# Kernel optimization log

Measured on AMD Instinct MI355X. Metric: run time of the kernel, lower is better.

Reference implementation:

```python
import jax, jax.numpy as jnp
import numpy as np

B, T, I, H = 2048, 512, 9, 56


def _lstm_layer(x, w_ih, w_hh, b_ih, b_hh):
    """Single LSTM layer, batch_first x: [B, T, in] -> [B, T, H].
    PyTorch gate order: i, f, g, o."""
    # Precompute input projections for all timesteps in one GEMM: [B, T, 4H]
    xp = jnp.einsum('bti,gi->btg', x, w_ih) + b_ih + b_hh
    xp_t = jnp.transpose(xp, (1, 0, 2))  # [T, B, 4H]
    h0 = jnp.zeros((x.shape[0], w_hh.shape[1]), dtype=x.dtype)
    c0 = jnp.zeros_like(h0)

    def step(carry, xt):
        h, c = carry
        gates = xt + h @ w_hh.T  # [B, 4H]
        i, f, g, o = jnp.split(gates, 4, axis=-1)
        i = jax.nn.sigmoid(i)
        f = jax.nn.sigmoid(f)
        g = jnp.tanh(g)
        o = jax.nn.sigmoid(o)
        c = f * c + i * g
        h = o * jnp.tanh(c)
        return (h, c), h

    _, hs = jax.lax.scan(step, (h0, c0), xp_t)  # hs: [T, B, H]
    return jnp.transpose(hs, (1, 0, 2))  # [B, T, H]


def setup_inputs() -> dict:
    key = jax.random.key(0)
    ks = jax.random.split(key, 13)
    s_in = 1.0 / np.sqrt(H)
    inp = {
        'x': jax.random.normal(ks[0], (B, T, I), dtype=jnp.float32),
        'w_ih0': jax.random.uniform(ks[1], (4 * H, I), jnp.float32, -s_in, s_in),
        'w_hh0': jax.random.uniform(ks[2], (4 * H, H), jnp.float32, -s_in, s_in),
        'b_ih0': jax.random.uniform(ks[3], (4 * H,), jnp.float32, -s_in, s_in),
        'b_hh0': jax.random.uniform(ks[4], (4 * H,), jnp.float32, -s_in, s_in),
        'w_ih1': jax.random.uniform(ks[5], (4 * H, H), jnp.float32, -s_in, s_in),
        'w_hh1': jax.random.uniform(ks[6], (4 * H, H), jnp.float32, -s_in, s_in),
        'b_ih1': jax.random.uniform(ks[7], (4 * H,), jnp.float32, -s_in, s_in),
        'b_hh1': jax.random.uniform(ks[8], (4 * H,), jnp.float32, -s_in, s_in),
        'fc1_w': jax.random.uniform(ks[9], (H // 2, H), jnp.float32, -s_in, s_in),
        'fc1_b': jax.random.uniform(ks[10], (H // 2,), jnp.float32, -s_in, s_in),
        'fc2_w': jax.random.uniform(ks[11], (1, H // 2), jnp.float32, -0.2, 0.2),
        'fc2_b': jax.random.uniform(ks[12], (1,), jnp.float32, -0.2, 0.2),
    }
    return inp


def reference(x, w_ih0, w_hh0, b_ih0, b_hh0, w_ih1, w_hh1, b_ih1, b_hh1,
              fc1_w, fc1_b, fc2_w, fc2_b):
    h = _lstm_layer(x, w_ih0, w_hh0, b_ih0, b_hh0)   # [B, T, H]
    h = _lstm_layer(h, w_ih1, w_hh1, b_ih1, b_hh1)   # [B, T, H]
    last = h[:, -1]                                   # [B, H]
    y = jax.nn.relu(last @ fc1_w.T + fc1_b)           # [B, H//2]
    return y @ fc2_w.T + fc2_b                        # [B, 1]
```

## Files before the change

kernel.cpp:

```cpp
#include <hip/hip_runtime.h>
#include <stdint.h>

#define T_LEN 512
#define IN0   9
#define H     56
#define BG    8
#define NW    14
#define NTH   (NW * 64)
#define NBLK  256

typedef __attribute__((ext_vector_type(8))) short bfrag;
typedef __attribute__((ext_vector_type(4))) float ffrag;

#define MFMA(a,b,c) __builtin_amdgcn_mfma_f32_16x16x32_bf16((a),(b),(c),0,0,0)

__device__ __forceinline__ uint32_t bf16hi(float x) {
  uint32_t u = __float_as_uint(x);
  return (u + 0x7FFFu + ((u >> 16) & 1u)) & 0xFFFF0000u;
}
__device__ __forceinline__ void split_bf16(float x, short& hs, short& ls) {
  uint32_t hb = bf16hi(x);
  float lf = x - __uint_as_float(hb);
  hs = (short)(hb >> 16);
  ls = (short)(bf16hi(lf) >> 16);
}
__device__ __forceinline__ void split_bf16t(float x, short& hs, short& ls) {
  uint32_t hb = bf16hi(x);
  float lf = x - __uint_as_float(hb);
  hs = (short)(hb >> 16);
  ls = (short)(__float_as_uint(lf) >> 16);
}
__device__ __forceinline__ float dpp8(float v) {
  return __int_as_float(__builtin_amdgcn_update_dpp(0, __float_as_int(v), 0x128, 0xF, 0xF, true));
}
__device__ __forceinline__ float rcp_f(float v)  { return __builtin_amdgcn_rcpf(v); }
__device__ __forceinline__ float sigm_f(float v) { return rcp_f(1.0f + __expf(-v)); }
__device__ __forceinline__ float tanh_f(float v) { return 1.0f - 2.0f * rcp_f(1.0f + __expf(2.0f * v)); }

__global__ __launch_bounds__(NTH, 4)
void lstm_mfma10(const float* __restrict__ x,
                 const float* __restrict__ w_ih0, const float* __restrict__ w_hh0,
                 const float* __restrict__ b_ih0, const float* __restrict__ b_hh0,
                 const float* __restrict__ w_ih1, const float* __restrict__ w_hh1,
                 const float* __restrict__ b_ih1, const float* __restrict__ b_hh1,
                 const float* __restrict__ fc1_w, const float* __restrict__ fc1_b,
                 const float* __restrict__ fc2_w, const float* __restrict__ fc2_b,
                 float* __restrict__ out)
{
  __shared__ __align__(16) short hbufS[4 * 1024];
  __shared__ __align__(16) short xfS[T_LEN * 128];
  __shared__ __align__(16) float x8S[T_LEN * BG];
  __shared__ float sF[BG * H];
  __shared__ float sY[BG * 28];

  const int tid  = threadIdx.x;
  const int lane = tid & 63;
  const int w    = tid >> 6;
  const int c16  = lane & 15;
  const int quad = lane >> 4;

  const int np   = 16 * w + c16;
  const int jb   = np >> 2, gb = np & 3;
  const int wrow = gb * H + jb;

  for (int i = tid; i < 2048; i += NTH) ((int*)hbufS)[i] = 0;

  bfrag B0h[2], B0l[2], Buh[2], Bhh[2];
  #pragma unroll
  for (int s = 0; s < 2; ++s) {
    union { short sh[8]; bfrag v; } a0h, a0l, auh, ahh;
    #pragma unroll
    for (int jj = 0; jj < 8; ++jj) {
      const int k = 32 * s + quad * 8 + jj;
      const float w0 = (k < H) ? w_hh0[wrow * H + k] : w_ih0[wrow * IN0 + (k - 56)];
      const float wu = (k < H) ? w_ih1[wrow * H + k] : 0.0f;
      const float wh = (k < H) ? w_hh1[wrow * H + k] : 0.0f;
      split_bf16(w0, a0h.sh[jj], a0l.sh[jj]);
      short dum;
      split_bf16(wu, auh.sh[jj], dum);
      split_bf16(wh, ahh.sh[jj], dum);
    }
    B0h[s] = a0h.v; B0l[s] = a0l.v;
    Buh[s] = auh.v; Bhh[s] = ahh.v;
  }

  const int j4 = 4 * w + quad;
  ffrag bias0f, bias1f;
  #pragma unroll
  for (int r = 0; r < 4; ++r) {
    const float v0 = b_ih0[r * H + j4] + b_hh0[r * H + j4];
    const float v1 = b_ih1[r * H + j4] + b_hh1[r * H + j4];
    bias0f[r] = (c16 < 8) ? v0 : 0.0f;
    bias1f[r] = (c16 < 8) ? v1 : 0.0f;
  }
  const ffrag zerof = { 0.f, 0.f, 0.f, 0.f };

  const int lay = (lane >> 3) & 1;
  const int b   = lane & 7;
  float wx8a[4];
  #pragma unroll
  for (int r = 0; r < 4; ++r)
    wx8a[r] = lay ? w_ih0[(r * H + j4) * IN0 + 8] : 0.0f;

  const int kk   = j4 & 31;
  const int offE = (j4 >> 5) * 512 + ((kk >> 3) * 16 + b) * 8 + (kk & 7);
  short* const hp0 = hbufS + (lay ? 0 : 3 * 1024) + offE;
  short* const hp1 = hbufS + (lay ? 1 * 1024 : 2 * 1024) + offE;

  for (int item = tid; item < T_LEN * BG; item += NTH) {
    const int t  = item & (T_LEN - 1);
    const int bb = item >> 9;
    const float* xr = x + ((size_t)(blockIdx.x * BG + bb) * T_LEN + t) * IN0;
    union { short s[8]; bfrag v; } hi, lo;
    #pragma unroll
    for (int q = 0; q < 8; ++q) split_bf16t(xr[q], hi.s[q], lo.s[q]);
    *(bfrag*)((char*)xfS + (size_t)t * 256 + bb * 16)       = hi.v;
    *(bfrag*)((char*)xfS + (size_t)t * 256 + (bb + 8) * 16) = lo.v;
    x8S[t * 8 + bb] = xr[8];
  }

  const char* const hB = (const char*)hbufS;
  const char* const pU0_0 = hB + 2048 + lane * 16;
  const char* const pU0_1 = hB +        lane * 16;
  const char* const pH0_0 = hB + 4096 + lane * 16;
  const char* const pH1_0 = hB + 5120 + lane * 16;
  const char* const pH0_1 = hB + 6144 + lane * 16;
  const char* const pH1_1 = hB + 7168 + lane * 16;
  const char* pU1_0 = (quad == 3) ? ((const char*)xfS + 256 * 1 + c16 * 16)
                                  : (hB + 3072 + lane * 16);
  const char* pU1_1 = (quad == 3) ? ((const char*)xfS + 256 * 2 + c16 * 16)
                                  : (hB + 1024 + lane * 16);
  const char* px8_0 = (const char*)x8S + 32 * 1 + b * 4;
  const char* px8_1 = (const char*)x8S + 32 * 2 + b * 4;
  const int incU1 = (quad == 3) ? 512 : 0;

  float cst = 0.f;
  __syncthreads();

  {
    const bfrag U0 = *(const bfrag*)(hB + lane * 16);
    const char* pU1p = (quad == 3) ? ((const char*)xfS + c16 * 16)
                                   : (hB + 1024 + lane * 16);
    const bfrag U1 = *(const bfrag*)pU1p;
    const float x8v = x8S[b];
    ffrag a0 = MFMA(B0h[0], U0, bias0f);
    a0 = MFMA(B0h[1], U1, a0);
    a0 = MFMA(B0l[0], U0, a0);
    a0 = MFMA(B0l[1], U1, a0);
    float s0[4];
    #pragma unroll
    for (int r = 0; r < 4; ++r) s0[r] = a0[r] + dpp8(a0[r]);
    if (lay) {
      const float gi = fmaf(wx8a[0], x8v, s0[0]);
      const float gf = fmaf(wx8a[1], x8v, s0[1]);
      const float gg = fmaf(wx8a[2], x8v, s0[2]);
      const float go = fmaf(wx8a[3], x8v, s0[3]);
      const float iv = sigm_f(gi), fv = sigm_f(gf);
      const float gv = tanh_f(gg), ov = sigm_f(go);
      cst = fmaf(fv, cst, iv * gv);
      const float hv = ov * tanh_f(cst);
      short hs, hl; split_bf16t(hv, hs, hl);
      hp1[0] = hs; hp1[64] = hl;
    }
    __syncthreads();
  }

#define REGION(RR, L0PART, LASTR)                                               \
  {                                                                             \
    const bfrag U0 = *(const bfrag*)pU0_##RR;                                   \
    const bfrag U1 = *(const bfrag*)pU1_##RR;                                   \
    const bfrag H0 = *(const bfrag*)pH0_##RR;                                   \
    const bfrag H1 = *(const bfrag*)pH1_##RR;                                   \
    ffrag a0a, a0b;                                                             \
    float x8v = 0.0f;                                                           \
    if (L0PART) x8v = *(const float*)px8_##RR;                                  \
    __builtin_amdgcn_s_setprio(1);                                              \
    if (L0PART) {                                                               \
                           \
      a0a = MFMA(B0h[0], U0, bias0f);                                           \
      a0b = MFMA(B0l[0], U0, zerof);                                            \
      a0a = MFMA(B0h[1], U1, a0a);                                              \
      a0b = MFMA(B0l[1], U1, a0b);                                              \
    }                                                                           \
          \
    ffrag aH = MFMA(Bhh[0], H0, bias1f);                                        \
    aH = MFMA(Bhh[1], H1, aH);                                                  \
    aH = MFMA(Buh[0], U0, aH);                                                  \
    aH = MFMA(Buh[1], U1, aH);                                                  \
    __builtin_amdgcn_s_setprio(0);                                              \
    if (!LASTR) {                                                               \
      \
      float sv[4];                                                              \
      _Pragma("unroll")                                                         \
      for (int r = 0; r < 4; ++r) {                                             \
        const float t0 = a0a[r] + a0b[r];                                       \
        const float uu = lay ? t0 : aH[r];                                      \
        const float vv = lay ? aH[r] : t0;                                      \
        sv[r] = uu + dpp8(vv);                                                  \
      }                                                                         \
      const float gi = fmaf(wx8a[0], x8v, sv[0]);                               \
      const float gf = fmaf(wx8a[1], x8v, sv[1]);                               \
      const float gg = fmaf(wx8a[2], x8v, sv[2]);                               \
      const float go = fmaf(wx8a[3], x8v, sv[3]);                               \
      const float iv = sigm_f(gi), fv = sigm_f(gf);                             \
      const float gv = tanh_f(gg), ov = sigm_f(go);                             \
      cst = fmaf(fv, cst, iv * gv);                                             \
      const float hv = ov * tanh_f(cst);                                        \
      short hs, hl; split_bf16t(hv, hs, hl);                                    \
      short* hb2 = (RR == 0) ? hp0 : hp1;                                       \
      hb2[0] = hs; hb2[64] = hl;                                                \
    } else {                                                                    \
      float s1[4];                                                              \
      _Pragma("unroll")                                                         \
      for (int r = 0; r < 4; ++r) s1[r] = aH[r] + dpp8(aH[r]);                  \
      if (lay == 0) {                                                           \
        const float iv = sigm_f(s1[0]), fv = sigm_f(s1[1]);                     \
        const float gv = tanh_f(s1[2]), ov = sigm_f(s1[3]);                     \
        cst = fmaf(fv, cst, iv * gv);                                           \
        sF[b * H + j4] = ov * tanh_f(cst);                                      \
      }                                                                         \
    }                                                                           \
    __syncthreads();                                                            \
  }

  for (int it = 0; it < 255; ++it) {
    REGION(0, 1, 0)
    REGION(1, 1, 0)
    pU1_0 += incU1; pU1_1 += incU1;
    px8_0 += 64;    px8_1 += 64;
  }
  REGION(0, 1, 0)
  pU1_1 -= incU1;
  REGION(1, 0, 1)
#undef REGION

  if (tid < 28 * BG) {
    const int m  = tid >> 3;
    const int bb = tid & 7;
    float acc = fc1_b[m];
    const float4* w4 = (const float4*)(fc1_w + m * H);
    const float4* h4 = (const float4*)(sF + bb * H);
    #pragma unroll
    for (int qq = 0; qq < H / 4; ++qq) {
      const float4 wv4 = w4[qq], hv4 = h4[qq];
      acc = fmaf(wv4.x, hv4.x, acc);
      acc = fmaf(wv4.y, hv4.y, acc);
      acc = fmaf(wv4.z, hv4.z, acc);
      acc = fmaf(wv4.w, hv4.w, acc);
    }
    sY[bb * 28 + m] = fmaxf(acc, 0.0f);
  }
  __syncthreads();
  if (tid < BG) {
    float acc = fc2_b[0];
    #pragma unroll
    for (int m = 0; m < 28; ++m)
      acc = fmaf(fc2_w[m], sY[tid * 28 + m], acc);
    out[blockIdx.x * BG + tid] = acc;
  }
}

extern "C" void kernel_launch(void* const* d_in, const int* in_sizes, int n_in,
                              void* d_out, int out_size, void* d_ws, size_t ws_size,
                              hipStream_t stream)
{
  const float* x     = (const float*)d_in[0];
  const float* w_ih0 = (const float*)d_in[1];
  const float* w_hh0 = (const float*)d_in[2];
  const float* b_ih0 = (const float*)d_in[3];
  const float* b_hh0 = (const float*)d_in[4];
  const float* w_ih1 = (const float*)d_in[5];
  const float* w_hh1 = (const float*)d_in[6];
  const float* b_ih1 = (const float*)d_in[7];
  const float* b_hh1 = (const float*)d_in[8];
  const float* fc1_w = (const float*)d_in[9];
  const float* fc1_b = (const float*)d_in[10];
  const float* fc2_w = (const float*)d_in[11];
  const float* fc2_b = (const float*)d_in[12];
  float* out = (float*)d_out;

  lstm_mfma10<<<NBLK, NTH, 0, stream>>>(
      x, w_ih0, w_hh0, b_ih0, b_hh0, w_ih1, w_hh1, b_ih1, b_hh1,
      fc1_w, fc1_b, fc2_w, fc2_b, out);
}
```

Baseline: 425.8 us.

## Cut waves per block from 14 to 8, each handling two gate slices

Each block now runs 8 wavefronts instead of 14. Waves 0-5 each own two 16-column weight slices (the second is slice 8+w), and waves 6-7 own one. The MFMA and activation work per wave roughly doubles for most waves, in exchange for fewer waves taking part in each per-timestep __syncthreads barrier and less per-block scheduling overhead. The costs are higher register pressure, since weight fragments are duplicated, and load imbalance between waves with one and two slices on the serial recurrence path.

```diff
diff --git a/kernel.cpp b/kernel.cpp
--- a/kernel.cpp
+++ b/kernel.cpp
@@ -5,7 +5,7 @@
 #define IN0   9
 #define H     56
 #define BG    8
-#define NW    14
+#define NW    8
 #define NTH   (NW * 64)
 #define NBLK  256
 
@@ -37,8 +37,8 @@
 __device__ __forceinline__ float sigm_f(float v) { return rcp_f(1.0f + __expf(-v)); }
 __device__ __forceinline__ float tanh_f(float v) { return 1.0f - 2.0f * rcp_f(1.0f + __expf(2.0f * v)); }
 
-__global__ __launch_bounds__(NTH, 4)
-void lstm_mfma10(const float* __restrict__ x,
+__global__ __launch_bounds__(NTH, 2)
+void lstm_mfma12(const float* __restrict__ x,
                  const float* __restrict__ w_ih0, const float* __restrict__ w_hh0,
                  const float* __restrict__ b_ih0, const float* __restrict__ b_hh0,
                  const float* __restrict__ w_ih1, const float* __restrict__ w_hh1,
@@ -59,53 +59,72 @@
   const int c16  = lane & 15;
   const int quad = lane >> 4;
 
-  const int np   = 16 * w + c16;
-  const int jb   = np >> 2, gb = np & 3;
-  const int wrow = gb * H + jb;
+  const bool HASB = (w < 6);
+  const int  sBi  = HASB ? (8 + w) : 0;
 
   for (int i = tid; i < 2048; i += NTH) ((int*)hbufS)[i] = 0;
-
-  bfrag B0h[2], B0l[2], Buh[2], Bhh[2];
-  #pragma unroll
-  for (int s = 0; s < 2; ++s) {
-    union { short sh[8]; bfrag v; } a0h, a0l, auh, ahh;
-    #pragma unroll
-    for (int jj = 0; jj < 8; ++jj) {
-      const int k = 32 * s + quad * 8 + jj;
-      const float w0 = (k < H) ? w_hh0[wrow * H + k] : w_ih0[wrow * IN0 + (k - 56)];
-      const float wu = (k < H) ? w_ih1[wrow * H + k] : 0.0f;
-      const float wh = (k < H) ? w_hh1[wrow * H + k] : 0.0f;
-      split_bf16(w0, a0h.sh[jj], a0l.sh[jj]);
-      short dum;
-      split_bf16(wu, auh.sh[jj], dum);
-      split_bf16(wh, ahh.sh[jj], dum);
-    }
-    B0h[s] = a0h.v; B0l[s] = a0l.v;
-    Buh[s] = auh.v; Bhh[s] = ahh.v;
-  }
-
-  const int j4 = 4 * w + quad;
-  ffrag bias0f, bias1f;
-  #pragma unroll
-  for (int r = 0; r < 4; ++r) {
-    const float v0 = b_ih0[r * H + j4] + b_hh0[r * H + j4];
-    const float v1 = b_ih1[r * H + j4] + b_hh1[r * H + j4];
-    bias0f[r] = (c16 < 8) ? v0 : 0.0f;
-    bias1f[r] = (c16 < 8) ? v1 : 0.0f;
-  }
-  const ffrag zerof = { 0.f, 0.f, 0.f, 0.f };
 
   const int lay = (lane >> 3) & 1;
   const int b   = lane & 7;
-  float wx8a[4];
-  #pragma unroll
-  for (int r = 0; r < 4; ++r)
-    wx8a[r] = lay ? w_ih0[(r * H + j4) * IN0 + 8] : 0.0f;
-
-  const int kk   = j4 & 31;
-  const int offE = (j4 >> 5) * 512 + ((kk >> 3) * 16 + b) * 8 + (kk & 7);
-  short* const hp0 = hbufS + (lay ? 0 : 3 * 1024) + offE;
-  short* const hp1 = hbufS + (lay ? 1 * 1024 : 2 * 1024) + offE;
+
+  bfrag B0hA[2], B0lA[2], BuhA[2], BhhA[2];
+  bfrag B0hB[2], B0lB[2], BuhB[2], BhhB[2];
+
+#define LOADA(SUF, SIDX)                                                        \
+  {                                                                             \
+    const int np_ = 16 * (SIDX) + c16;                                          \
+    const int jb_ = np_ >> 2, gb_ = np_ & 3;                                    \
+    const int wrow_ = gb_ * H + jb_;                                            \
+    _Pragma("unroll")                                                           \
+    for (int s = 0; s < 2; ++s) {                                               \
+      union { short sh[8]; bfrag v; } a0h, a0l, auh, ahh;                       \
+      _Pragma("unroll")                                                         \
+      for (int jj = 0; jj < 8; ++jj) {                                          \
+        const int k = 32 * s + quad * 8 + jj;                                   \
+        const float w0 = (k < H) ? w_hh0[wrow_ * H + k]                         \
+                                 : w_ih0[wrow_ * IN0 + (k - 56)];               \
+        const float wu = (k < H) ? w_ih1[wrow_ * H + k] : 0.0f;                 \
+        const float wh = (k < H) ? w_hh1[wrow_ * H + k] : 0.0f;                 \
+        split_bf16(w0, a0h.sh[jj], a0l.sh[jj]);                                 \
+        short dum;                                                              \
+        split_bf16(wu, auh.sh[jj], dum);                       \
+        split_bf16(wh, ahh.sh[jj], dum);                                        \
+      }                                                                         \
+      B0h##SUF[s] = a0h.v; B0l##SUF[s] = a0l.v;                                 \
+      Buh##SUF[s] = auh.v; Bhh##SUF[s] = ahh.v;                                 \
+    }                                                                           \
+  }
+
+  LOADA(A, w)
+  LOADA(B, sBi)
+#undef LOADA
+
+  const int j4A = 4 * w + quad;
+  const int j4B = 4 * sBi + quad;
+  const ffrag zerof = { 0.f, 0.f, 0.f, 0.f };
+
+#define SETUPS(SUF, J4)                                                         \
+  ffrag bias0f##SUF, bias1f##SUF;                                               \
+  _Pragma("unroll")                                                             \
+  for (int r = 0; r < 4; ++r) {                                                 \
+    const float v0 = b_ih0[r * H + (J4)] + b_hh0[r * H + (J4)];                 \
+    const float v1 = b_ih1[r * H + (J4)] + b_hh1[r * H + (J4)];                 \
+    bias0f##SUF[r] = (c16 < 8) ? v0 : 0.0f;                                     \
+    bias1f##SUF[r] = (c16 < 8) ? v1 : 0.0f;                                     \
+  }                                                                             \
+  float wx8a##SUF[4];                                                           \
+  _Pragma("unroll")                                                             \
+  for (int r = 0; r < 4; ++r)                                                   \
+    wx8a##SUF[r] = lay ? w_ih0[(r * H + (J4)) * IN0 + 8] : 0.0f;                \
+  const int kk##SUF = (J4) & 31;                                                \
+  const int offE##SUF = ((J4) >> 5) * 512 + ((kk##SUF >> 3) * 16 + b) * 8       \
+                        + (kk##SUF & 7);                                        \
+  short* const hp0##SUF = hbufS + (lay ? 0 : 3 * 1024) + offE##SUF;             \
+  short* const hp1##SUF = hbufS + (lay ? 1 * 1024 : 2 * 1024) + offE##SUF;
+
+  SETUPS(A, j4A)
+  SETUPS(B, j4B)
+#undef SETUPS
 
   for (int item = tid; item < T_LEN * BG; item += NTH) {
     const int t  = item & (T_LEN - 1);
@@ -134,8 +153,62 @@
   const char* px8_1 = (const char*)x8S + 32 * 2 + b * 4;
   const int incU1 = (quad == 3) ? 512 : 0;
 
-  float cst = 0.f;
+  float cstA = 0.f, cstB = 0.f;
   __syncthreads();
+
+#define ACT0(A0, WX8, CST, HBP, X8V)                                            \
+  {                                                                             \
+    float s0[4];                                                                \
+    _Pragma("unroll")                                                           \
+    for (int r = 0; r < 4; ++r) s0[r] = A0[r] + dpp8(A0[r]);                    \
+    if (lay) {                                                                  \
+      const float gi = fmaf(WX8[0], X8V, s0[0]);                                \
+      const float gf = fmaf(WX8[1], X8V, s0[1]);                                \
+      const float gg = fmaf(WX8[2], X8V, s0[2]);                                \
+      const float go = fmaf(WX8[3], X8V, s0[3]);                                \
+      const float iv = sigm_f(gi), fv = sigm_f(gf);                             \
+      const float gv = tanh_f(gg), ov = sigm_f(go);                             \
+      CST = fmaf(fv, CST, iv * gv);                                             \
+      const float hv = ov * tanh_f(CST);                                        \
+      short hs, hl; split_bf16t(hv, hs, hl);                                    \
+      (HBP)[0] = hs; (HBP)[64] = hl;                                            \
+    }                                                                           \
+  }
+
+#define ACT1(A0A, A0B, AH, WX8, CST, HBP, X8V)                                  \
+  {                                                                             \
+    float sv[4];                                                                \
+    _Pragma("unroll")                                                           \
+    for (int r = 0; r < 4; ++r) {                                               \
+      const float t0 = A0A[r] + A0B[r];                                         \
+      const float uu = lay ? t0 : AH[r];                                        \
+      const float vv = lay ? AH[r] : t0;                                        \
+      sv[r] = uu + dpp8(vv);                                                    \
+    }                                                                           \
+    const float gi = fmaf(WX8[0], X8V, sv[0]);                                  \
+    const float gf = fmaf(WX8[1], X8V, sv[1]);                                  \
+    const float gg = fmaf(WX8[2], X8V, sv[2]);                                  \
+    const float go = fmaf(WX8[3], X8V, sv[3]);                                  \
+    const float iv = sigm_f(gi), fv = sigm_f(gf);                               \
+    const float gv = tanh_f(gg), ov = sigm_f(go);                               \
+    CST = fmaf(fv, CST, iv * gv);                                               \
+    const float hv = ov * tanh_f(CST);                                          \
+    short hs, hl; split_bf16t(hv, hs, hl);                                      \
+    (HBP)[0] = hs; (HBP)[64] = hl;                                              \
+  }
+
+#define ACTL(AH, CST, J4)                                                       \
+  {                                                                             \
+    float s1[4];                                                                \
+    _Pragma("unroll")                                                           \
+    for (int r = 0; r < 4; ++r) s1[r] = AH[r] + dpp8(AH[r]);                    \
+    if (lay == 0) {                                                             \
+      const float iv = sigm_f(s1[0]), fv = sigm_f(s1[1]);                       \
+      const float gv = tanh_f(s1[2]), ov = sigm_f(s1[3]);                       \
+      CST = fmaf(fv, CST, iv * gv);                                             \
+      sF[b * H + (J4)] = ov * tanh_f(CST);                                      \
+    }                                                                           \
+  }
 
   {
     const bfrag U0 = *(const bfrag*)(hB + lane * 16);
@@ -143,24 +216,17 @@
                                    : (hB + 1024 + lane * 16);
     const bfrag U1 = *(const bfrag*)pU1p;
     const float x8v = x8S[b];
-    ffrag a0 = MFMA(B0h[0], U0, bias0f);
-    a0 = MFMA(B0h[1], U1, a0);
-    a0 = MFMA(B0l[0], U0, a0);
-    a0 = MFMA(B0l[1], U1, a0);
-    float s0[4];
-    #pragma unroll
-    for (int r = 0; r < 4; ++r) s0[r] = a0[r] + dpp8(a0[r]);
-    if (lay) {
-      const float gi = fmaf(wx8a[0], x8v, s0[0]);
-      const float gf = fmaf(wx8a[1], x8v, s0[1]);
-      const float gg = fmaf(wx8a[2], x8v, s0[2]);
-      const float go = fmaf(wx8a[3], x8v, s0[3]);
-      const float iv = sigm_f(gi), fv = sigm_f(gf);
-      const float gv = tanh_f(gg), ov = sigm_f(go);
-      cst = fmaf(fv, cst, iv * gv);
-      const float hv = ov * tanh_f(cst);
-      short hs, hl; split_bf16t(hv, hs, hl);
-      hp1[0] = hs; hp1[64] = hl;
+    ffrag a0A = MFMA(B0hA[0], U0, bias0fA);
+    a0A = MFMA(B0hA[1], U1, a0A);
+    a0A = MFMA(B0lA[0], U0, a0A);
+    a0A = MFMA(B0lA[1], U1, a0A);
+    ACT0(a0A, wx8aA, cstA, hp1A, x8v)
+    if (HASB) {
+      ffrag a0B = MFMA(B0hB[0], U0, bias0fB);
+      a0B = MFMA(B0hB[1], U1, a0B);
+      a0B = MFMA(B0lB[0], U0, a0B);
+      a0B = MFMA(B0lB[1], U1, a0B);
+      ACT0(a0B, wx8aB, cstB, hp1B, x8v)
     }
     __syncthreads();
   }
@@ -171,54 +237,43 @@
     const bfrag U1 = *(const bfrag*)pU1_##RR;                                   \
     const bfrag H0 = *(const bfrag*)pH0_##RR;                                   \
     const bfrag H1 = *(const bfrag*)pH1_##RR;                                   \
-    ffrag a0a, a0b;                                                             \
+    ffrag a0aA, a0bA, a0aB, a0bB;                                               \
     float x8v = 0.0f;                                                           \
     if (L0PART) x8v = *(const float*)px8_##RR;                                  \
     __builtin_amdgcn_s_setprio(1);                                              \
     if (L0PART) {                                                               \
-                           \
-      a0a = MFMA(B0h[0], U0, bias0f);                                           \
-      a0b = MFMA(B0l[0], U0, zerof);                                            \
-      a0a = MFMA(B0h[1], U1, a0a);                                              \
-      a0b = MFMA(B0l[1], U1, a0b);                                              \
+      a0aA = MFMA(B0hA[0], U0, bias0fA);                                        \
+      a0bA = MFMA(B0lA[0], U0, zerof);                                          \
+      a0aA = MFMA(B0hA[1], U1, a0aA);                                           \
+      a0bA = MFMA(B0lA[1], U1, a0bA);                                           \
+      if (HASB) {                                                               \
+        a0aB = MFMA(B0hB[0], U0, bias0fB);                                      \
+        a0bB = MFMA(B0lB[0], U0, zerof);                                        \
+        a0aB = MFMA(B0hB[1], U1, a0aB);                                         \
+        a0bB = MFMA(B0lB[1], U1, a0bB);                                         \
+      }                                                                         \
     }                                                                           \
           \
-    ffrag aH = MFMA(Bhh[0], H0, bias1f);                                        \
-    aH = MFMA(Bhh[1], H1, aH);                                                  \
-    aH = MFMA(Buh[0], U0, aH);                                                  \
-    aH = MFMA(Buh[1], U1, aH);                                                  \
+    ffrag aHA = MFMA(BhhA[0], H0, bias1fA);                                     \
+    aHA = MFMA(BhhA[1], H1, aHA);                                               \
+    aHA = MFMA(BuhA[0], U0, aHA);                                               \
+    aHA = MFMA(BuhA[1], U1, aHA);                                               \
+    ffrag aHB;                                                                  \
+    if (HASB) {                                                                 \
+      aHB = MFMA(BhhB[0], H0, bias1fB);                                         \
+      aHB = MFMA(BhhB[1], H1, aHB);                                             \
+      aHB = MFMA(BuhB[0], U0, aHB);                                             \
+      aHB = MFMA(BuhB[1], U1, aHB);                                             \
+    }                                                                           \
     __builtin_amdgcn_s_setprio(0);                                              \
     if (!LASTR) {                                                               \
-      \
-      float sv[4];                                                              \
-      _Pragma("unroll")                                                         \
-      for (int r = 0; r < 4; ++r) {                                             \
-        const float t0 = a0a[r] + a0b[r];                                       \
-        const float uu = lay ? t0 : aH[r];                                      \
-        const float vv = lay ? aH[r] : t0;                                      \
-        sv[r] = uu + dpp8(vv);                                                  \
+      ACT1(a0aA, a0bA, aHA, wx8aA, cstA, ((RR) == 0) ? hp0A : hp1A, x8v)        \
+      if (HASB) {                                                               \
+        ACT1(a0aB, a0bB, aHB, wx8aB, cstB, ((RR) == 0) ? hp0B : hp1B, x8v)      \
       }                                                                         \
-      const float gi = fmaf(wx8a[0], x8v, sv[0]);                               \
-      const float gf = fmaf(wx8a[1], x8v, sv[1]);                               \
-      const float gg = fmaf(wx8a[2], x8v, sv[2]);                               \
-      const float go = fmaf(wx8a[3], x8v, sv[3]);                               \
-      const float iv = sigm_f(gi), fv = sigm_f(gf);                             \
-      const float gv = tanh_f(gg), ov = sigm_f(go);                             \
-      cst = fmaf(fv, cst, iv * gv);                                             \
-      const float hv = ov * tanh_f(cst);                                        \
-      short hs, hl; split_bf16t(hv, hs, hl);                                    \
-      short* hb2 = (RR == 0) ? hp0 : hp1;                                       \
-      hb2[0] = hs; hb2[64] = hl;                                                \
     } else {                                                                    \
-      float s1[4];                                                              \
-      _Pragma("unroll")                                                         \
-      for (int r = 0; r < 4; ++r) s1[r] = aH[r] + dpp8(aH[r]);                  \
-      if (lay == 0) {                                                           \
-        const float iv = sigm_f(s1[0]), fv = sigm_f(s1[1]);                     \
-        const float gv = tanh_f(s1[2]), ov = sigm_f(s1[3]);                     \
-        cst = fmaf(fv, cst, iv * gv);                                           \
-        sF[b * H + j4] = ov * tanh_f(cst);                                      \
-      }                                                                         \
+      ACTL(aHA, cstA, j4A)                                                      \
+      if (HASB) { ACTL(aHB, cstB, j4B) }                                        \
     }                                                                           \
     __syncthreads();                                                            \
   }
@@ -233,6 +288,9 @@
   pU1_1 -= incU1;
   REGION(1, 0, 1)
 #undef REGION
+#undef ACT0
+#undef ACT1
+#undef ACTL
 
   if (tid < 28 * BG) {
     const int m  = tid >> 3;
@@ -279,7 +337,7 @@
   const float* fc2_b = (const float*)d_in[12];
   float* out = (float*)d_out;
 
-  lstm_mfma10<<<NBLK, NTH, 0, stream>>>(
+  lstm_mfma12<<<NBLK, NTH, 0, stream>>>(
       x, w_ih0, w_hh0, b_ih0, b_hh0, w_ih1, w_hh1, b_ih1, b_hh1,
       fc1_w, fc1_b, fc2_w, fc2_b, out);
 }
```

Measured after the change: 476.1 us. 11.8% more time.

## Split layers across wave groups with LDS flag handshakes instead of block barriers

Applied to the files above, without the earlier changes.

Before, all 14 waves computed both layers in lockstep, with a __syncthreads after every timestep. Now waves 0-6 run layer 0 and waves 7-13 run layer 1, each wave handling two 16-column slices. The groups exchange h through LDS double buffers and sync through per-step atomic counters with spin-wait and sleep. This lets layer 1 lag layer 0 by one step without a block-wide barrier. It risks extra spin latency, and the wait has a guard timeout that could silently break ordering if it expires.

```diff
diff --git a/kernel.cpp b/kernel.cpp
--- a/kernel.cpp
+++ b/kernel.cpp
@@ -37,8 +37,20 @@
 __device__ __forceinline__ float sigm_f(float v) { return rcp_f(1.0f + __expf(-v)); }
 __device__ __forceinline__ float tanh_f(float v) { return 1.0f - 2.0f * rcp_f(1.0f + __expf(2.0f * v)); }
 
+__device__ __forceinline__ int ftgt(int s) { return (s < 0) ? 0 : 7 * ((s >> 3) + 1); }
+
+__device__ __forceinline__ void wait_flag(const int* f, int tgt) {
+  if (tgt <= 0) return;
+  const volatile int* vf = (const volatile int*)f;
+  if (*vf < tgt) {
+    int guard = 1 << 13;
+    do { __builtin_amdgcn_s_sleep(2); } while (*vf < tgt && --guard);
+  }
+  asm volatile("" ::: "memory");
+}
+
 __global__ __launch_bounds__(NTH, 4)
-void lstm_mfma10(const float* __restrict__ x,
+void lstm_mfma13(const float* __restrict__ x,
                  const float* __restrict__ w_ih0, const float* __restrict__ w_hh0,
                  const float* __restrict__ b_ih0, const float* __restrict__ b_hh0,
                  const float* __restrict__ w_ih1, const float* __restrict__ w_hh1,
@@ -52,6 +64,7 @@
   __shared__ __align__(16) float x8S[T_LEN * BG];
   __shared__ float sF[BG * H];
   __shared__ float sY[BG * 28];
+  __shared__ int   flg[16];
 
   const int tid  = threadIdx.x;
   const int lane = tid & 63;
@@ -59,53 +72,18 @@
   const int c16  = lane & 15;
   const int quad = lane >> 4;
 
-  const int np   = 16 * w + c16;
-  const int jb   = np >> 2, gb = np & 3;
-  const int wrow = gb * H + jb;
+  const int  grp  = (w >= 7);
+  const int  wg   = grp ? (w - 7) : w;
+  const bool selB = (c16 >= 8);
+  const int  b    = lane & 7;
+  const int  sA   = 2 * wg, sB = 2 * wg + 1;
+  const int  j_sel = 4 * (selB ? sB : sA) + quad;
 
   for (int i = tid; i < 2048; i += NTH) ((int*)hbufS)[i] = 0;
-
-  bfrag B0h[2], B0l[2], Buh[2], Bhh[2];
-  #pragma unroll
-  for (int s = 0; s < 2; ++s) {
-    union { short sh[8]; bfrag v; } a0h, a0l, auh, ahh;
-    #pragma unroll
-    for (int jj = 0; jj < 8; ++jj) {
-      const int k = 32 * s + quad * 8 + jj;
-      const float w0 = (k < H) ? w_hh0[wrow * H + k] : w_ih0[wrow * IN0 + (k - 56)];
-      const float wu = (k < H) ? w_ih1[wrow * H + k] : 0.0f;
-      const float wh = (k < H) ? w_hh1[wrow * H + k] : 0.0f;
-      split_bf16(w0, a0h.sh[jj], a0l.sh[jj]);
-      short dum;
-      split_bf16(wu, auh.sh[jj], dum);
-      split_bf16(wh, ahh.sh[jj], dum);
-    }
-    B0h[s] = a0h.v; B0l[s] = a0l.v;
-    Buh[s] = auh.v; Bhh[s] = ahh.v;
-  }
-
-  const int j4 = 4 * w + quad;
-  ffrag bias0f, bias1f;
-  #pragma unroll
-  for (int r = 0; r < 4; ++r) {
-    const float v0 = b_ih0[r * H + j4] + b_hh0[r * H + j4];
-    const float v1 = b_ih1[r * H + j4] + b_hh1[r * H + j4];
-    bias0f[r] = (c16 < 8) ? v0 : 0.0f;
-    bias1f[r] = (c16 < 8) ? v1 : 0.0f;
-  }
-  const ffrag zerof = { 0.f, 0.f, 0.f, 0.f };
-
-  const int lay = (lane >> 3) & 1;
-  const int b   = lane & 7;
-  float wx8a[4];
-  #pragma unroll
-  for (int r = 0; r < 4; ++r)
-    wx8a[r] = lay ? w_ih0[(r * H + j4) * IN0 + 8] : 0.0f;
-
-  const int kk   = j4 & 31;
-  const int offE = (j4 >> 5) * 512 + ((kk >> 3) * 16 + b) * 8 + (kk & 7);
-  short* const hp0 = hbufS + (lay ? 0 : 3 * 1024) + offE;
-  short* const hp1 = hbufS + (lay ? 1 * 1024 : 2 * 1024) + offE;
+  if (tid < 16) flg[tid] = 0;
+
+  const int kk   = j_sel & 31;
+  const int offE = (j_sel >> 5) * 512 + ((kk >> 3) * 16 + b) * 8 + (kk & 7);
 
   for (int item = tid; item < T_LEN * BG; item += NTH) {
     const int t  = item & (T_LEN - 1);
@@ -119,120 +97,202 @@
     x8S[t * 8 + bb] = xr[8];
   }
 
-  const char* const hB = (const char*)hbufS;
-  const char* const pU0_0 = hB + 2048 + lane * 16;
-  const char* const pU0_1 = hB +        lane * 16;
-  const char* const pH0_0 = hB + 4096 + lane * 16;
-  const char* const pH1_0 = hB + 5120 + lane * 16;
-  const char* const pH0_1 = hB + 6144 + lane * 16;
-  const char* const pH1_1 = hB + 7168 + lane * 16;
-  const char* pU1_0 = (quad == 3) ? ((const char*)xfS + 256 * 1 + c16 * 16)
-                                  : (hB + 3072 + lane * 16);
-  const char* pU1_1 = (quad == 3) ? ((const char*)xfS + 256 * 2 + c16 * 16)
-                                  : (hB + 1024 + lane * 16);
-  const char* px8_0 = (const char*)x8S + 32 * 1 + b * 4;
-  const char* px8_1 = (const char*)x8S + 32 * 2 + b * 4;
+  const char* const ldsb = (const char*)hbufS;
+  const char* const xfb  = (const char*)xfS;
+  const ffrag zerof = { 0.f, 0.f, 0.f, 0.f };
   const int incU1 = (quad == 3) ? 512 : 0;
-
   float cst = 0.f;
+
   __syncthreads();
 
-  {
-    const bfrag U0 = *(const bfrag*)(hB + lane * 16);
-    const char* pU1p = (quad == 3) ? ((const char*)xfS + c16 * 16)
-                                   : (hB + 1024 + lane * 16);
-    const bfrag U1 = *(const bfrag*)pU1p;
-    const float x8v = x8S[b];
-    ffrag a0 = MFMA(B0h[0], U0, bias0f);
-    a0 = MFMA(B0h[1], U1, a0);
-    a0 = MFMA(B0l[0], U0, a0);
-    a0 = MFMA(B0l[1], U1, a0);
-    float s0[4];
-    #pragma unroll
-    for (int r = 0; r < 4; ++r) s0[r] = a0[r] + dpp8(a0[r]);
-    if (lay) {
-      const float gi = fmaf(wx8a[0], x8v, s0[0]);
-      const float gf = fmaf(wx8a[1], x8v, s0[1]);
-      const float gg = fmaf(wx8a[2], x8v, s0[2]);
-      const float go = fmaf(wx8a[3], x8v, s0[3]);
-      const float iv = sigm_f(gi), fv = sigm_f(gf);
-      const float gv = tanh_f(gg), ov = sigm_f(go);
-      cst = fmaf(fv, cst, iv * gv);
-      const float hv = ov * tanh_f(cst);
-      short hs, hl; split_bf16t(hv, hs, hl);
-      hp1[0] = hs; hp1[64] = hl;
-    }
-    __syncthreads();
-  }
-
-#define REGION(RR, L0PART, LASTR)                                               \
-  {                                                                             \
-    const bfrag U0 = *(const bfrag*)pU0_##RR;                                   \
-    const bfrag U1 = *(const bfrag*)pU1_##RR;                                   \
-    const bfrag H0 = *(const bfrag*)pH0_##RR;                                   \
-    const bfrag H1 = *(const bfrag*)pH1_##RR;                                   \
-    ffrag a0a, a0b;                                                             \
-    float x8v = 0.0f;                                                           \
-    if (L0PART) x8v = *(const float*)px8_##RR;                                  \
-    __builtin_amdgcn_s_setprio(1);                                              \
-    if (L0PART) {                                                               \
-                           \
-      a0a = MFMA(B0h[0], U0, bias0f);                                           \
-      a0b = MFMA(B0l[0], U0, zerof);                                            \
-      a0a = MFMA(B0h[1], U1, a0a);                                              \
-      a0b = MFMA(B0l[1], U1, a0b);                                              \
-    }                                                                           \
-          \
-    ffrag aH = MFMA(Bhh[0], H0, bias1f);                                        \
-    aH = MFMA(Bhh[1], H1, aH);                                                  \
-    aH = MFMA(Buh[0], U0, aH);                                                  \
-    aH = MFMA(Buh[1], U1, aH);                                                  \
-    __builtin_amdgcn_s_setprio(0);                                              \
-    if (!LASTR) {                                                               \
-      \
+#define SIGNAL(IDX8, STEP)                                                      \
+  asm volatile("s_waitcnt lgkmcnt(0)" ::: "memory");                            \
+  if (lane == 0) atomicAdd(&flg[(IDX8) + ((STEP) & 7)], 1);
+
+  if (!grp) {
+    bfrag B0hA[2], B0lA[2], B0hB[2], B0lB[2];
+#define LOADW0(SUF, SIDX)                                                       \
+    {                                                                           \
+      const int np_ = 16 * (SIDX) + c16;                                        \
+      const int wrow_ = (np_ & 3) * H + (np_ >> 2);                             \
+      _Pragma("unroll")                                                         \
+      for (int s = 0; s < 2; ++s) {                                             \
+        union { short sh[8]; bfrag v; } ah, al;                                 \
+        _Pragma("unroll")                                                       \
+        for (int jj = 0; jj < 8; ++jj) {                                        \
+          const int k = 32 * s + quad * 8 + jj;                                 \
+          const float w0 = (k < H) ? w_hh0[wrow_ * H + k]                       \
+                                   : w_ih0[wrow_ * IN0 + (k - 56)];             \
+          split_bf16(w0, ah.sh[jj], al.sh[jj]);                                 \
+        }                                                                       \
+        B0h##SUF[s] = ah.v; B0l##SUF[s] = al.v;                                 \
+      }                                                                         \
+    }
+    LOADW0(A, sA)
+    LOADW0(B, sB)
+#undef LOADW0
+
+    ffrag bias0A, bias0B;
+    #pragma unroll
+    for (int r = 0; r < 4; ++r) {
+      const int jA = 4 * sA + quad, jB = 4 * sB + quad;
+      bias0A[r] = (c16 < 8) ? (b_ih0[r * H + jA] + b_hh0[r * H + jA]) : 0.0f;
+      bias0B[r] = (c16 < 8) ? (b_ih0[r * H + jB] + b_hh0[r * H + jB]) : 0.0f;
+    }
+    float wx8s[4];
+    #pragma unroll
+    for (int r = 0; r < 4; ++r)
+      wx8s[r] = w_ih0[(r * H + j_sel) * IN0 + 8];
+
+    const char* const pU0_0 = ldsb + 2048 + lane * 16;
+    const char* const pU0_1 = ldsb +        lane * 16;
+    const char* pU1_0 = (quad == 3) ? (xfb +       c16 * 16) : (ldsb + 3072 + lane * 16);
+    const char* pU1_1 = (quad == 3) ? (xfb + 256 + c16 * 16) : (ldsb + 1024 + lane * 16);
+    const char* px8_0 = (const char*)x8S +      b * 4;
+    const char* px8_1 = (const char*)x8S + 32 + b * 4;
+    short* const hw_0 = hbufS +        offE;
+    short* const hw_1 = hbufS + 1024 + offE;
+
+#define STEP0(P, TT)                                                            \
+    {                                                                           \
+      const float x8v = *(const float*)px8_##P;                                 \
+      wait_flag(&flg[((TT) - 1) & 7], ftgt((TT) - 1));                          \
+      wait_flag(&flg[8 + (((TT) - 2) & 7)], ftgt((TT) - 2));                    \
+      const bfrag U0 = *(const bfrag*)pU0_##P;                                  \
+      const bfrag U1 = *(const bfrag*)pU1_##P;                                  \
+      __builtin_amdgcn_s_setprio(1);                                            \
+      ffrag aA = MFMA(B0hA[0], U0, bias0A);                                     \
+      ffrag bA = MFMA(B0lA[0], U0, zerof);                                      \
+      aA = MFMA(B0hA[1], U1, aA);                                               \
+      bA = MFMA(B0lA[1], U1, bA);                                               \
+      ffrag aB = MFMA(B0hB[0], U0, bias0B);                                     \
+      ffrag bB = MFMA(B0lB[0], U0, zerof);                                      \
+      aB = MFMA(B0hB[1], U1, aB);                                               \
+      bB = MFMA(B0lB[1], U1, bB);                                               \
+      __builtin_amdgcn_s_setprio(0);                                            \
       float sv[4];                                                              \
       _Pragma("unroll")                                                         \
       for (int r = 0; r < 4; ++r) {                                             \
-        const float t0 = a0a[r] + a0b[r];                                       \
-        const float uu = lay ? t0 : aH[r];                                      \
-        const float vv = lay ? aH[r] : t0;                                      \
+        const float da = aA[r] + bA[r];                                         \
+        const float db = aB[r] + bB[r];                                         \
+        const float uu = selB ? db : da;                                        \
+        const float vv = selB ? da : db;                                        \
         sv[r] = uu + dpp8(vv);                                                  \
       }                                                                         \
-      const float gi = fmaf(wx8a[0], x8v, sv[0]);                               \
-      const float gf = fmaf(wx8a[1], x8v, sv[1]);                               \
-      const float gg = fmaf(wx8a[2], x8v, sv[2]);                               \
-      const float go = fmaf(wx8a[3], x8v, sv[3]);                               \
+      const float gi = fmaf(wx8s[0], x8v, sv[0]);                               \
+      const float gf = fmaf(wx8s[1], x8v, sv[1]);                               \
+      const float gg = fmaf(wx8s[2], x8v, sv[2]);                               \
+      const float go = fmaf(wx8s[3], x8v, sv[3]);                               \
       const float iv = sigm_f(gi), fv = sigm_f(gf);                             \
       const float gv = tanh_f(gg), ov = sigm_f(go);                             \
       cst = fmaf(fv, cst, iv * gv);                                             \
       const float hv = ov * tanh_f(cst);                                        \
       short hs, hl; split_bf16t(hv, hs, hl);                                    \
-      short* hb2 = (RR == 0) ? hp0 : hp1;                                       \
-      hb2[0] = hs; hb2[64] = hl;                                                \
-    } else {                                                                    \
-      float s1[4];                                                              \
+      hw_##P[0] = hs; hw_##P[64] = hl;                                          \
+      SIGNAL(0, TT)                                                             \
+    }
+
+    for (int t = 0; t < T_LEN; t += 2) {
+      STEP0(0, t)
+      STEP0(1, t + 1)
+      pU1_0 += incU1; pU1_1 += incU1;
+      px8_0 += 64;    px8_1 += 64;
+    }
+#undef STEP0
+  } else {
+    bfrag BuhA[2], BhhA[2], BuhB[2], BhhB[2];
+#define LOADW1(SUF, SIDX)                                                       \
+    {                                                                           \
+      const int np_ = 16 * (SIDX) + c16;                                        \
+      const int wrow_ = (np_ & 3) * H + (np_ >> 2);                             \
       _Pragma("unroll")                                                         \
-      for (int r = 0; r < 4; ++r) s1[r] = aH[r] + dpp8(aH[r]);                  \
-      if (lay == 0) {                                                           \
-        const float iv = sigm_f(s1[0]), fv = sigm_f(s1[1]);                     \
-        const float gv = tanh_f(s1[2]), ov = sigm_f(s1[3]);                     \
-        cst = fmaf(fv, cst, iv * gv);                                           \
-        sF[b * H + j4] = ov * tanh_f(cst);                                      \
-      }                                                                         \
-    }                                                                           \
-    __syncthreads();                                                            \
-  }
-
-  for (int it = 0; it < 255; ++it) {
-    REGION(0, 1, 0)
-    REGION(1, 1, 0)
-    pU1_0 += incU1; pU1_1 += incU1;
-    px8_0 += 64;    px8_1 += 64;
-  }
-  REGION(0, 1, 0)
-  pU1_1 -= incU1;
-  REGION(1, 0, 1)
-#undef REGION
+      for (int s = 0; s < 2; ++s) {                                             \
+        union { short sh[8]; bfrag v; } au, ah;                                 \
+        _Pragma("unroll")                                                       \
+        for (int jj = 0; jj < 8; ++jj) {                                        \
+          const int k = 32 * s + quad * 8 + jj;                                 \
+          const float wu = (k < H) ? w_ih1[wrow_ * H + k] : 0.0f;               \
+          const float wh = (k < H) ? w_hh1[wrow_ * H + k] : 0.0f;               \
+          short dum;                                                            \
+          split_bf16(wu, au.sh[jj], dum);                      \
+          split_bf16(wh, ah.sh[jj], dum);                                       \
+        }                                                                       \
+        Buh##SUF[s] = au.v; Bhh##SUF[s] = ah.v;                                 \
+      }                                                                         \
+    }
+    LOADW1(A, sA)
+    LOADW1(B, sB)
+#undef LOADW1
+
+    ffrag bias1A, bias1B;
+    #pragma unroll
+    for (int r = 0; r < 4; ++r) {
+      const int jA = 4 * sA + quad, jB = 4 * sB + quad;
+      bias1A[r] = (c16 < 8) ? (b_ih1[r * H + jA] + b_hh1[r * H + jA]) : 0.0f;
+      bias1B[r] = (c16 < 8) ? (b_ih1[r * H + jB] + b_hh1[r * H + jB]) : 0.0f;
+    }
+
+    const char* const qU0_0 = ldsb +        lane * 16;
+    const char* const qU0_1 = ldsb + 2048 + lane * 16;
+    const char* qU1_0 = (quad == 3) ? (xfb +       c16 * 16) : (ldsb + 1024 + lane * 16);
+    const char* qU1_1 = (quad == 3) ? (xfb + 256 + c16 * 16) : (ldsb + 3072 + lane * 16);
+    const char* const qH0_0 = ldsb + 4096 + 2048 + lane * 16;
+    const char* const qH1_0 = qH0_0 + 1024;
+    const char* const qH0_1 = ldsb + 4096 +        lane * 16;
+    const char* const qH1_1 = qH0_1 + 1024;
+    short* const qw_0 = hbufS + 2 * 1024 + offE;
+    short* const qw_1 = hbufS + 3 * 1024 + offE;
+
+#define STEP1(P, SS, LAST)                                                      \
+    {                                                                           \
+      wait_flag(&flg[(SS) & 7], ftgt(SS));                                      \
+      wait_flag(&flg[8 + (((SS) - 1) & 7)], ftgt((SS) - 1));                    \
+      const bfrag U0 = *(const bfrag*)qU0_##P;                                  \
+      const bfrag U1 = *(const bfrag*)qU1_##P;                                  \
+      const bfrag H0 = *(const bfrag*)qH0_##P;                                  \
+      const bfrag H1 = *(const bfrag*)qH1_##P;                                  \
+      __builtin_amdgcn_s_setprio(1);                                            \
+      ffrag hA = MFMA(BhhA[0], H0, bias1A);                                     \
+      hA = MFMA(BhhA[1], H1, hA);                                               \
+      hA = MFMA(BuhA[0], U0, hA);                                               \
+      hA = MFMA(BuhA[1], U1, hA);                                               \
+      ffrag hBv = MFMA(BhhB[0], H0, bias1B);                                    \
+      hBv = MFMA(BhhB[1], H1, hBv);                                             \
+      hBv = MFMA(BuhB[0], U0, hBv);                                             \
+      hBv = MFMA(BuhB[1], U1, hBv);                                             \
+      __builtin_amdgcn_s_setprio(0);                                            \
+      float sv[4];                                                              \
+      _Pragma("unroll")                                                         \
+      for (int r = 0; r < 4; ++r) {                                             \
+        const float uu = selB ? hBv[r] : hA[r];                                 \
+        const float vv = selB ? hA[r] : hBv[r];                                 \
+        sv[r] = uu + dpp8(vv);                                                  \
+      }                                                                         \
+      const float iv = sigm_f(sv[0]), fv = sigm_f(sv[1]);                       \
+      const float gv = tanh_f(sv[2]), ov = sigm_f(sv[3]);                       \
+      cst = fmaf(fv, cst, iv * gv);                                             \
+      const float hv = ov * tanh_f(cst);                                        \
+      if (!(LAST)) {                                                            \
+        short hs, hl; split_bf16t(hv, hs, hl);                                  \
+        qw_##P[0] = hs; qw_##P[64] = hl;                                        \
+        SIGNAL(8, SS)                                                           \
+      } else {                                                                  \
+        sF[b * H + j_sel] = hv;                                                 \
+      }                                                                         \
+    }
+
+    for (int s = 0; s < T_LEN - 2; s += 2) {
+      STEP1(0, s, 0)
+      STEP1(1, s + 1, 0)
+      qU1_0 += incU1; qU1_1 += incU1;
+    }
+    STEP1(0, T_LEN - 2, 0)
+    STEP1(1, T_LEN - 1, 1)
+#undef STEP1
+  }
+#undef SIGNAL
+
+  __syncthreads();
 
   if (tid < 28 * BG) {
     const int m  = tid >> 3;
@@ -279,7 +339,7 @@
   const float* fc2_b = (const float*)d_in[12];
   float* out = (float*)d_out;
 
-  lstm_mfma10<<<NBLK, NTH, 0, stream>>>(
+  lstm_mfma13<<<NBLK, NTH, 0, stream>>>(
       x, w_ih0, w_hh0, b_ih0, b_hh0, w_ih1, w_hh1, b_ih1, b_hh1,
       fc1_w, fc1_b, fc2_w, fc2_b, out);
 }
```

Measured after the change: 495.0 us. 1.16x slower.
